# Kernel optimization log

Measured on AMD Instinct MI355X. Metric: run time of the kernel, lower is better.

## Reference

```python
import jax, jax.numpy as jnp
import numpy as np

B, IN, OUT, NC = 4096, 256, 256, 8  # batch, in_dim, out_dim, n_coef


def jacobi_design_matrix(t, alpha, beta, n_coefs):
    """Jacobi polynomials P_0..P_{n-1}(t) via three-term recurrence; t: [..., ]."""
    polys = [jnp.ones_like(t)]
    if n_coefs > 1:
        polys.append((alpha + 1.0) + (alpha + beta + 2.0) * (t - 1.0) * 0.5)
    for n in range(2, n_coefs):
        c = 2.0 * n + alpha + beta
        A = 2.0 * n * (n + alpha + beta) * (c - 2.0)
        Bc = (c - 1.0) * (c * (c - 2.0) * t + alpha * alpha - beta * beta)
        Cc = 2.0 * (n + alpha - 1.0) * (n + beta - 1.0) * c
        polys.append((Bc * polys[-1] - Cc * polys[-2]) / A)
    return jnp.stack(polys, axis=-1)  # [..., n_coefs]


def setup_inputs() -> dict:
    key = jax.random.key(0)
    k1, k2, k3, k4, k5 = jax.random.split(key, 5)
    return {
        "x": jax.random.normal(k1, (B, IN), jnp.float32),
        "coefs": jax.random.normal(k2, (IN, OUT, NC), jnp.float32) * 0.03,
        "alpha_arctanh": jax.random.normal(k3, (), jnp.float32) * 0.1,
        "resid_scale": jax.random.normal(k4, (IN, 1), jnp.float32),
        "spline_scale": jax.random.normal(k5, (IN, OUT), jnp.float32) * 0.1,
    }


def reference(x, coefs, alpha_arctanh, resid_scale, spline_scale):
    alpha = jnp.tanh(alpha_arctanh)
    # spline input map = tanh; design matrix per input element: [B, in, NC]
    dm = jacobi_design_matrix(jnp.tanh(x), alpha, alpha, NC)
    # coefs einsum 'ic,ioc->io' (batched): [B, in, out]
    y = jnp.einsum('bic,ioc->bio', dm, coefs)
    # residual branch (base_act = tanh) + spline scale; dropout is identity (rate 0, deterministic)
    y = resid_scale[None] * jnp.tanh(x)[..., None] + spline_scale[None] * y
    # mean over in_dim -> [B, out]
    return jnp.mean(y, axis=1)
```

## Files before the change

kernel.cpp:

```cpp
#include <hip/hip_runtime.h>
#include <hip/hip_bf16.h>

#define B_SZ 4096
#define IN_D 256
#define OUT_D 256
#define NC 8

#define BM 64
#define BN 32
#define SSTEPS 16

using f32x4 = __attribute__((ext_vector_type(4))) float;
using s16x8 = __attribute__((ext_vector_type(8))) short;

__device__ __forceinline__ unsigned short f2bf(float f) {
    union { float f; unsigned int u; } v; v.f = f;
    return (unsigned short)((v.u + 0x7fffu + ((v.u >> 16) & 1u)) >> 16);
}

__device__ __forceinline__ float fast_tanh(float x) {
    float e = __expf(2.0f * x);
    return 1.0f - 2.0f / (e + 1.0f);
}

__global__ __launch_bounds__(256) void kan_prep(
    const float* __restrict__ x, const float* __restrict__ coefs,
    const float* __restrict__ alpha_at, const float* __restrict__ resid_scale,
    const float* __restrict__ spline_scale,
    float* __restrict__ tT, unsigned short* __restrict__ Wg)
{
    const int tid = threadIdx.x;

    if (blockIdx.x < 512) {
        __shared__ float tt[32][65];
        const int bid = blockIdx.x;
        const int b0 = (bid & 127) * 32;
        const int i0 = (bid >> 7) * 64;
        #pragma unroll
        for (int it = 0; it < 8; it++) {
            int e = it * 256 + tid;
            int r = e >> 6, c = e & 63;
            tt[r][c] = fast_tanh(x[(size_t)(b0 + r) * IN_D + i0 + c]);
        }
        __syncthreads();
        #pragma unroll
        for (int it = 0; it < 8; it++) {
            int e = it * 256 + tid;
            int ii = e >> 5, bb = e & 31;
            tT[(size_t)(i0 + ii) * B_SZ + b0 + bb] = tt[bb][ii];
        }
        return;
    }

    const int i = blockIdx.x - 512;
    const int o = tid;

    float al = tanhf(alpha_at[0]);
    float mono[NC][NC];
    #pragma unroll
    for (int a = 0; a < NC; a++)
        #pragma unroll
        for (int b = 0; b < NC; b++) mono[a][b] = 0.f;
    mono[0][0] = 1.f;
    mono[1][1] = al + 1.f;
    #pragma unroll
    for (int n = 2; n < NC; n++) {
        float fn = (float)n;
        float c  = 2.f * fn + 2.f * al;
        float An = 2.f * fn * (fn + 2.f * al) * (c - 2.f);
        float Bn = (c - 1.f) * c * (c - 2.f);
        float Cn = 2.f * (fn + al - 1.f) * (fn + al - 1.f) * c;
        #pragma unroll
        for (int j = 0; j < NC; j++) {
            float tm = (j > 0 ? mono[n - 1][j - 1] : 0.f);
            mono[n][j] = (Bn * tm - Cn * mono[n - 2][j]) / An;
        }
    }

    float cf[NC];
    const float* cp = coefs + ((size_t)i * OUT_D + o) * NC;
    #pragma unroll
    for (int c = 0; c < NC; c++) cf[c] = cp[c];
    float ss = spline_scale[i * OUT_D + o];
    float rs = resid_scale[i];

    unsigned short w8[NC];
    #pragma unroll
    for (int j = 0; j < NC; j++) {
        float wv = 0.f;
        #pragma unroll
        for (int c = 0; c < NC; c++) wv += mono[c][j] * cf[c];
        wv *= ss * (1.0f / IN_D);
        if (j == 1) wv += rs * (1.0f / IN_D);
        w8[j] = f2bf(wv);
    }
    uint4 pk;
    unsigned int* pu = (unsigned int*)&pk;
    #pragma unroll
    for (int h = 0; h < 4; h++)
        pu[h] = (unsigned int)w8[2 * h] | ((unsigned int)w8[2 * h + 1] << 16);
    *(uint4*)(Wg + ((size_t)i * OUT_D + o) * NC) = pk;
}

__global__ __launch_bounds__(256) void kan_gemm(
    const float* __restrict__ tT, const unsigned short* __restrict__ Wg,
    float* __restrict__ out)
{
    __shared__ __align__(16) float lbuf[3][64 * 36];

    const int tid  = threadIdx.x;
    const int lane = tid & 63;
    const int kg   = tid >> 6;
    const int lr   = lane & 15;
    const int il   = lane >> 4;

    const int bid  = blockIdx.x;
    const int swz  = (bid & 7) * 64 + (bid >> 3);
    const int mblk = swz >> 3, nblk = swz & 7;
    const int bm = mblk * BM, bn = nblk * BN;

    f32x4 acc[4][2];
    #pragma unroll
    for (int f = 0; f < 4; f++)
        #pragma unroll
        for (int g = 0; g < 2; g++)
            acc[f][g] = (f32x4){0.f, 0.f, 0.f, 0.f};

    #pragma unroll 4
    for (int s = 0; s < SSTEPS; ++s) {
        const int i0 = kg * 64 + s * 4 + il;

        uint4 bw[2];
        #pragma unroll
        for (int g = 0; g < 2; g++)
            bw[g] = *(const uint4*)(Wg + ((size_t)i0 * OUT_D + bn + g * 16 + lr) * 8);

        s16x8 af[4];
        #pragma unroll
        for (int f = 0; f < 4; f++) {
            float t = tT[(size_t)i0 * B_SZ + bm + f * 16 + lr];
            float p2 = t * t, p3 = p2 * t, p4 = p3 * t;
            float p5 = p4 * t, p6 = p5 * t, p7 = p6 * t;
            __hip_bfloat162 h0 = __float22bfloat162_rn(make_float2(1.0f, t));
            __hip_bfloat162 h1 = __float22bfloat162_rn(make_float2(p2, p3));
            __hip_bfloat162 h2 = __float22bfloat162_rn(make_float2(p4, p5));
            __hip_bfloat162 h3 = __float22bfloat162_rn(make_float2(p6, p7));
            uint4 pk;
            pk.x = *(unsigned int*)&h0;
            pk.y = *(unsigned int*)&h1;
            pk.z = *(unsigned int*)&h2;
            pk.w = *(unsigned int*)&h3;
            af[f] = *(s16x8*)&pk;
        }

        #pragma unroll
        for (int f = 0; f < 4; f++)
            #pragma unroll
            for (int g = 0; g < 2; g++)
                acc[f][g] = __builtin_amdgcn_mfma_f32_16x16x32_bf16(
                    af[f], *(s16x8*)&bw[g], acc[f][g], 0, 0, 0);
    }

    if (kg > 0) {
        float* dst = &lbuf[kg - 1][lane * 36];
        #pragma unroll
        for (int f = 0; f < 4; f++)
            #pragma unroll
            for (int g = 0; g < 2; g++)
                *(f32x4*)(dst + f * 8 + g * 4) = acc[f][g];
    }
    __syncthreads();
    if (kg == 0) {
        #pragma unroll
        for (int r = 0; r < 3; r++) {
            const float* src = &lbuf[r][lane * 36];
            #pragma unroll
            for (int f = 0; f < 4; f++)
                #pragma unroll
                for (int g = 0; g < 2; g++)
                    acc[f][g] += *(const f32x4*)(src + f * 8 + g * 4);
        }
        #pragma unroll
        for (int f = 0; f < 4; f++)
            #pragma unroll
            for (int g = 0; g < 2; g++)
                #pragma unroll
                for (int j = 0; j < 4; j++) {
                    int r = bm + f * 16 + il * 4 + j;
                    int c = bn + g * 16 + lr;
                    out[(size_t)r * OUT_D + c] = acc[f][g][j];
                }
    }
}

extern "C" void kernel_launch(void* const* d_in, const int* in_sizes, int n_in,
                              void* d_out, int out_size, void* d_ws, size_t ws_size,
                              hipStream_t stream) {
    const float* x     = (const float*)d_in[0];
    const float* coefs = (const float*)d_in[1];
    const float* alpha = (const float*)d_in[2];
    const float* rs    = (const float*)d_in[3];
    const float* ss    = (const float*)d_in[4];
    float* out = (float*)d_out;

    unsigned short* Wg = (unsigned short*)d_ws;
    float* tT = (float*)((char*)d_ws + (1 << 20));

    kan_prep<<<dim3(768), dim3(256), 0, stream>>>(x, coefs, alpha, rs, ss, tT, Wg);
    kan_gemm<<<dim3((B_SZ / BM) * (OUT_D / BN)), dim3(256), 0, stream>>>(tT, Wg, out);
}
```

Baseline: 20.58 us.

## Fuse tanh and transpose of x into the GEMM kernel via shared memory

The tanh-and-transpose stage moves out of the prep kernel and into kan_gemm. Each block loads its 64x256 tile of x, applies tanh, and stores it transposed in LDS (stride 68), so the tT round trip through global memory goes away. The prep kernel now only builds the weights, and the main loop is fully unrolled. In exchange, tanh is recomputed redundantly across the 8 N-blocks that share an M tile, the kernel uses about 68KB of LDS, which lowers occupancy, and each thread holds 64 registers for the tile load.

```diff
diff --git a/kernel.cpp b/kernel.cpp
--- a/kernel.cpp
+++ b/kernel.cpp
@@ -9,6 +9,7 @@
 #define BM 64
 #define BN 32
 #define SSTEPS 16
+#define TSTRIDE 68
 
 using f32x4 = __attribute__((ext_vector_type(4))) float;
 using s16x8 = __attribute__((ext_vector_type(8))) short;
@@ -23,37 +24,13 @@
     return 1.0f - 2.0f / (e + 1.0f);
 }
 
-__global__ __launch_bounds__(256) void kan_prep(
-    const float* __restrict__ x, const float* __restrict__ coefs,
-    const float* __restrict__ alpha_at, const float* __restrict__ resid_scale,
-    const float* __restrict__ spline_scale,
-    float* __restrict__ tT, unsigned short* __restrict__ Wg)
+__global__ __launch_bounds__(256) void prep_w(
+    const float* __restrict__ coefs, const float* __restrict__ alpha_at,
+    const float* __restrict__ resid_scale, const float* __restrict__ spline_scale,
+    unsigned short* __restrict__ Wg)
 {
-    const int tid = threadIdx.x;
-
-    if (blockIdx.x < 512) {
-        __shared__ float tt[32][65];
-        const int bid = blockIdx.x;
-        const int b0 = (bid & 127) * 32;
-        const int i0 = (bid >> 7) * 64;
-        #pragma unroll
-        for (int it = 0; it < 8; it++) {
-            int e = it * 256 + tid;
-            int r = e >> 6, c = e & 63;
-            tt[r][c] = fast_tanh(x[(size_t)(b0 + r) * IN_D + i0 + c]);
-        }
-        __syncthreads();
-        #pragma unroll
-        for (int it = 0; it < 8; it++) {
-            int e = it * 256 + tid;
-            int ii = e >> 5, bb = e & 31;
-            tT[(size_t)(i0 + ii) * B_SZ + b0 + bb] = tt[bb][ii];
-        }
-        return;
-    }
-
-    const int i = blockIdx.x - 512;
-    const int o = tid;
+    const int i = blockIdx.x;
+    const int o = threadIdx.x;
 
     float al = tanhf(alpha_at[0]);
     float mono[NC][NC];
@@ -103,10 +80,11 @@
 }
 
 __global__ __launch_bounds__(256) void kan_gemm(
-    const float* __restrict__ tT, const unsigned short* __restrict__ Wg,
+    const float* __restrict__ x, const unsigned short* __restrict__ Wg,
     float* __restrict__ out)
 {
-    __shared__ __align__(16) float lbuf[3][64 * 36];
+    __shared__ __align__(16) float smem[IN_D * TSTRIDE];
+    float* lbuf = smem;
 
     const int tid  = threadIdx.x;
     const int lane = tid & 63;
@@ -119,6 +97,21 @@
     const int mblk = swz >> 3, nblk = swz & 7;
     const int bm = mblk * BM, bn = nblk * BN;
 
+    {
+        const int i = tid;
+        float t[64];
+        #pragma unroll
+        for (int r = 0; r < 64; r++)
+            t[r] = fast_tanh(x[(size_t)(bm + r) * IN_D + i]);
+        float* row = smem + i * TSTRIDE;
+        #pragma unroll
+        for (int k = 0; k < 16; k++) {
+            f32x4 w4 = {t[k], t[k + 16], t[k + 32], t[k + 48]};
+            *(f32x4*)(row + 4 * k) = w4;
+        }
+    }
+    __syncthreads();
+
     f32x4 acc[4][2];
     #pragma unroll
     for (int f = 0; f < 4; f++)
@@ -126,7 +119,7 @@
         for (int g = 0; g < 2; g++)
             acc[f][g] = (f32x4){0.f, 0.f, 0.f, 0.f};
 
-    #pragma unroll 4
+    #pragma unroll
     for (int s = 0; s < SSTEPS; ++s) {
         const int i0 = kg * 64 + s * 4 + il;
 
@@ -135,10 +128,12 @@
         for (int g = 0; g < 2; g++)
             bw[g] = *(const uint4*)(Wg + ((size_t)i0 * OUT_D + bn + g * 16 + lr) * 8);
 
+        f32x4 tv = *(const f32x4*)(smem + i0 * TSTRIDE + lr * 4);
+
         s16x8 af[4];
         #pragma unroll
         for (int f = 0; f < 4; f++) {
-            float t = tT[(size_t)i0 * B_SZ + bm + f * 16 + lr];
+            float t = tv[f];
             float p2 = t * t, p3 = p2 * t, p4 = p3 * t;
             float p5 = p4 * t, p6 = p5 * t, p7 = p6 * t;
             __hip_bfloat162 h0 = __float22bfloat162_rn(make_float2(1.0f, t));
@@ -161,8 +156,9 @@
                     af[f], *(s16x8*)&bw[g], acc[f][g], 0, 0, 0);
     }
 
+    __syncthreads();
     if (kg > 0) {
-        float* dst = &lbuf[kg - 1][lane * 36];
+        float* dst = &lbuf[(kg - 1) * 64 * 36 + lane * 36];
         #pragma unroll
         for (int f = 0; f < 4; f++)
             #pragma unroll
@@ -173,7 +169,7 @@
     if (kg == 0) {
         #pragma unroll
         for (int r = 0; r < 3; r++) {
-            const float* src = &lbuf[r][lane * 36];
+            const float* src = &lbuf[r * 64 * 36 + lane * 36];
             #pragma unroll
             for (int f = 0; f < 4; f++)
                 #pragma unroll
@@ -204,8 +200,7 @@
     float* out = (float*)d_out;
 
     unsigned short* Wg = (unsigned short*)d_ws;
-    float* tT = (float*)((char*)d_ws + (1 << 20));
-
-    kan_prep<<<dim3(768), dim3(256), 0, stream>>>(x, coefs, alpha, rs, ss, tT, Wg);
-    kan_gemm<<<dim3((B_SZ / BM) * (OUT_D / BN)), dim3(256), 0, stream>>>(tT, Wg, out);
-}
+
+    prep_w<<<dim3(IN_D), dim3(OUT_D), 0, stream>>>(coefs, alpha, rs, ss, Wg);
+    kan_gemm<<<dim3((B_SZ / BM) * (OUT_D / BN)), dim3(256), 0, stream>>>(x, Wg, out);
+}
```

Measured after the change: 23.64 us. 1.15x slower.

## Interleave transposed tanh buffer so GEMM loads four batch values per vector load

Applied to the files above, without the earlier changes.

The prep kernel now writes tanh(x) transposed with the batch dimension interleaved in groups of four, so each GEMM lane fetches its four M-fragment values with one 16-byte load instead of four scalar loads. Prep tiles grow to 64x64, which cuts the transpose block count in half, and the GEMM main loop is fully unrolled with hoisted base pointers. The costs are a more complex index mapping, more register pressure from full unrolling, and a larger shared tile in prep.

```diff
diff --git a/kernel.cpp b/kernel.cpp
--- a/kernel.cpp
+++ b/kernel.cpp
@@ -27,32 +27,34 @@
     const float* __restrict__ x, const float* __restrict__ coefs,
     const float* __restrict__ alpha_at, const float* __restrict__ resid_scale,
     const float* __restrict__ spline_scale,
-    float* __restrict__ tT, unsigned short* __restrict__ Wg)
+    float* __restrict__ tTI, unsigned short* __restrict__ Wg)
 {
     const int tid = threadIdx.x;
-
-    if (blockIdx.x < 512) {
-        __shared__ float tt[32][65];
-        const int bid = blockIdx.x;
-        const int b0 = (bid & 127) * 32;
-        const int i0 = (bid >> 7) * 64;
-        #pragma unroll
-        for (int it = 0; it < 8; it++) {
+    const int bid = blockIdx.x;
+
+    if (bid < 256) {
+        __shared__ float tt[64][68];
+        const int b0 = (bid & 63) * 64;
+        const int i0 = (bid >> 6) * 64;
+        #pragma unroll
+        for (int it = 0; it < 16; it++) {
             int e = it * 256 + tid;
             int r = e >> 6, c = e & 63;
             tt[r][c] = fast_tanh(x[(size_t)(b0 + r) * IN_D + i0 + c]);
         }
         __syncthreads();
-        #pragma unroll
-        for (int it = 0; it < 8; it++) {
-            int e = it * 256 + tid;
-            int ii = e >> 5, bb = e & 31;
-            tT[(size_t)(i0 + ii) * B_SZ + b0 + bb] = tt[bb][ii];
+        const int lr = tid & 15;
+        const int ib = tid >> 4;
+        #pragma unroll
+        for (int k = 0; k < 4; k++) {
+            int i = ib + k * 16;
+            f32x4 v = { tt[lr][i], tt[lr + 16][i], tt[lr + 32][i], tt[lr + 48][i] };
+            *(f32x4*)(tTI + (size_t)(i0 + i) * B_SZ + b0 + lr * 4) = v;
         }
         return;
     }
 
-    const int i = blockIdx.x - 512;
+    const int i = bid - 256;
     const int o = tid;
 
     float al = tanhf(alpha_at[0]);
@@ -103,7 +105,7 @@
 }
 
 __global__ __launch_bounds__(256) void kan_gemm(
-    const float* __restrict__ tT, const unsigned short* __restrict__ Wg,
+    const float* __restrict__ tTI, const unsigned short* __restrict__ Wg,
     float* __restrict__ out)
 {
     __shared__ __align__(16) float lbuf[3][64 * 36];
@@ -126,19 +128,24 @@
         for (int g = 0; g < 2; g++)
             acc[f][g] = (f32x4){0.f, 0.f, 0.f, 0.f};
 
-    #pragma unroll 4
+    const float* tbase = tTI + bm + lr * 4;
+    const unsigned short* wbase = Wg + ((size_t)bn + lr) * NC;
+
+    #pragma unroll
     for (int s = 0; s < SSTEPS; ++s) {
         const int i0 = kg * 64 + s * 4 + il;
 
         uint4 bw[2];
         #pragma unroll
         for (int g = 0; g < 2; g++)
-            bw[g] = *(const uint4*)(Wg + ((size_t)i0 * OUT_D + bn + g * 16 + lr) * 8);
+            bw[g] = *(const uint4*)(wbase + ((size_t)i0 * OUT_D + g * 16) * NC);
+
+        f32x4 tv = *(const f32x4*)(tbase + (size_t)i0 * B_SZ);
 
         s16x8 af[4];
         #pragma unroll
         for (int f = 0; f < 4; f++) {
-            float t = tT[(size_t)i0 * B_SZ + bm + f * 16 + lr];
+            float t = tv[f];
             float p2 = t * t, p3 = p2 * t, p4 = p3 * t;
             float p5 = p4 * t, p6 = p5 * t, p7 = p6 * t;
             __hip_bfloat162 h0 = __float22bfloat162_rn(make_float2(1.0f, t));
@@ -204,8 +211,8 @@
     float* out = (float*)d_out;
 
     unsigned short* Wg = (unsigned short*)d_ws;
-    float* tT = (float*)((char*)d_ws + (1 << 20));
-
-    kan_prep<<<dim3(768), dim3(256), 0, stream>>>(x, coefs, alpha, rs, ss, tT, Wg);
-    kan_gemm<<<dim3((B_SZ / BM) * (OUT_D / BN)), dim3(256), 0, stream>>>(tT, Wg, out);
-}
+    float* tTI = (float*)((char*)d_ws + (1 << 20));
+
+    kan_prep<<<dim3(512), dim3(256), 0, stream>>>(x, coefs, alpha, rs, ss, tTI, Wg);
+    kan_gemm<<<dim3((B_SZ / BM) * (OUT_D / BN)), dim3(256), 0, stream>>>(tTI, Wg, out);
+}
```

New measurement: 19.93 us. -3.1%, faster.
